# Kernel optimization log

Hardware: AMD Instinct MI355X
Metric: run time of the kernel (lower is better)

Reference implementation:

```python
import jax, jax.numpy as jnp
import numpy as np

N_NODES = 100000
N_EDGES = 1600000
N_GRAPHS = 128
BEHAVIOR_DIM = 32
LLM_DIM = 768
LLM_PROJ = 32
HIDDEN = 64
NUM_CLASSES = 2
INPUT_DIM = 64 + 16 + LLM_PROJ + BEHAVIOR_DIM  # 144


def gcn_conv(h, edge_index, edge_weight, W, b, n):
    """PyG GCNConv: linear -> gcn_norm with self-loops -> scatter-add at target."""
    h = h @ W  # [N, out]
    row, col = edge_index[0], edge_index[1]
    loop = jnp.arange(n)
    row_f = jnp.concatenate([row, loop])
    col_f = jnp.concatenate([col, loop])
    ew_f = jnp.concatenate([edge_weight, jnp.ones((n,), h.dtype)])
    deg = jax.ops.segment_sum(ew_f, col_f, num_segments=n)
    dinv = jnp.where(deg > 0, jax.lax.rsqrt(deg), 0.0)
    norm = dinv[row_f] * ew_f * dinv[col_f]  # [E+N]
    out = jax.ops.segment_sum(norm[:, None] * h[row_f], col_f, num_segments=n)
    return out + b


def global_mean_pool(x, batch, num_graphs):
    s = jax.ops.segment_sum(x, batch, num_segments=num_graphs)
    cnt = jax.ops.segment_sum(jnp.ones((x.shape[0],), x.dtype), batch, num_segments=num_graphs)
    return s / jnp.maximum(cnt, 1.0)[:, None]


def setup_inputs() -> dict:
    key = jax.random.key(0)
    ks = jax.random.split(key, 16)
    inp = {
        "x_names": jax.random.randint(ks[0], (N_NODES,), 0, 20000),
        "x_types": jax.random.randint(ks[1], (N_NODES,), 0, 100),
        "x_behaviors": jax.random.normal(ks[2], (N_NODES, BEHAVIOR_DIM), jnp.float32),
        "edge_index": jax.random.randint(ks[3], (2, N_EDGES), 0, N_NODES),
        "edge_weight": jax.random.uniform(ks[4], (N_EDGES,), jnp.float32),
        "batch": jnp.sort(jax.random.randint(ks[5], (N_NODES,), 0, N_GRAPHS)),
        "llm_features": jax.random.normal(ks[6], (N_NODES, LLM_DIM), jnp.float32),
        # parameters
        "name_emb": jax.random.normal(ks[7], (20000, 64), jnp.float32),
        "type_emb": jax.random.normal(ks[8], (100, 16), jnp.float32),
        "llm_proj_w": jax.random.normal(ks[9], (LLM_DIM, LLM_PROJ), jnp.float32) * 0.02,
        "llm_proj_b": jnp.zeros((LLM_PROJ,), jnp.float32),
        "conv1_w": jax.random.normal(ks[10], (INPUT_DIM, HIDDEN), jnp.float32) * 0.08,
        "conv1_b": jnp.zeros((HIDDEN,), jnp.float32),
        "conv2_w": jax.random.normal(ks[11], (HIDDEN, HIDDEN), jnp.float32) * 0.12,
        "conv2_b": jnp.zeros((HIDDEN,), jnp.float32),
        "cls_w": jax.random.normal(ks[12], (HIDDEN, NUM_CLASSES), jnp.float32) * 0.12,
        "cls_b": jnp.zeros((NUM_CLASSES,), jnp.float32),
    }
    return inp


def reference(x_names, x_types, x_behaviors, edge_index, edge_weight, batch,
              llm_features, name_emb, type_emb, llm_proj_w, llm_proj_b,
              conv1_w, conv1_b, conv2_w, conv2_b, cls_w, cls_b):
    n = x_names.shape[0]
    name_feat = name_emb[x_names]          # [N, 64]
    type_feat = type_emb[x_types]          # [N, 16]
    llm_feat = llm_features @ llm_proj_w + llm_proj_b  # [N, 32]
    x = jnp.concatenate([name_feat, type_feat, llm_feat, x_behaviors], axis=1)
    # dropout is identity in eval mode
    x = jax.nn.relu(gcn_conv(x, edge_index, edge_weight, conv1_w, conv1_b, n))
    x = jax.nn.relu(gcn_conv(x, edge_index, edge_weight, conv2_w, conv2_b, n))
    x = global_mean_pool(x, batch, N_GRAPHS)  # [G, HIDDEN]
    return x @ cls_w + cls_b                   # [G, 2]
```

## Files before the change

### kernel.cpp

```cpp
#include <hip/hip_runtime.h>
#include <cstdint>
#include <cstddef>

typedef __attribute__((ext_vector_type(8))) short bf16x8;
typedef __attribute__((ext_vector_type(4))) float f32x4;


__device__ __forceinline__ unsigned bf_rne(float x) {
  unsigned u = __float_as_uint(x);
  return (u + 0x7FFFu + ((u >> 16) & 1u)) >> 16;
}

__device__ __forceinline__ void split1(float x, short& hi, short& lo) {
  unsigned hb = bf_rne(x);
  hi = (short)hb;
  float fh = __uint_as_float(hb << 16);
  lo = (short)bf_rne(x - fh);
}

__device__ __forceinline__ void split8(const float4& p, const float4& q, bf16x8& h, bf16x8& l) {
  short hh, ll;
  split1(p.x, hh, ll); h[0] = hh; l[0] = ll;
  split1(p.y, hh, ll); h[1] = hh; l[1] = ll;
  split1(p.z, hh, ll); h[2] = hh; l[2] = ll;
  split1(p.w, hh, ll); h[3] = hh; l[3] = ll;
  split1(q.x, hh, ll); h[4] = hh; l[4] = ll;
  split1(q.y, hh, ll); h[5] = hh; l[5] = ll;
  split1(q.z, hh, ll); h[6] = hh; l[6] = ll;
  split1(q.w, hh, ll); h[7] = hh; l[7] = ll;
}


__global__ void prep1_kernel(const float* __restrict__ pw, const float* __restrict__ pb,
                             const float* __restrict__ w1,
                             short* __restrict__ Bh, short* __restrict__ Bl,
                             float* __restrict__ biasf) {
  int idx = blockIdx.x * 256 + threadIdx.x;
  if (idx < 896 * 64) {
    int gk = idx >> 6, col = idx & 63;
    float val;
    if (gk < 768) {
      float acc = 0.0f;
      #pragma unroll 8
      for (int m = 0; m < 32; ++m) acc = fmaf(pw[gk * 32 + m], w1[(80 + m) * 64 + col], acc);
      val = acc;
    } else if (gk < 832) val = w1[(gk - 768) * 64 + col];
    else if (gk < 848)   val = w1[(64 + gk - 832) * 64 + col];
    else if (gk < 864)   val = w1[(112 + gk - 848) * 64 + col];
    else if (gk < 880)   val = w1[(128 + gk - 864) * 64 + col];
    else                 val = 0.0f;
    int chunk = gk >> 5, k = gk & 31;
    int g, j;
    if (k < 16) { g = k >> 2; j = k & 3; } else { int k2 = k - 16; g = k2 >> 2; j = 4 + (k2 & 3); }
    size_t o = ((size_t)(chunk * 4 + g) * 64 + col) * 8 + j;
    short hh, ll; split1(val, hh, ll);
    Bh[o] = hh; Bl[o] = ll;
  } else if (idx < 896 * 64 + 64) {
    int col = idx - 896 * 64;
    float acc = 0.0f;
    for (int m = 0; m < 32; ++m) acc = fmaf(pb[m], w1[(80 + m) * 64 + col], acc);
    biasf[col] = acc;
  }
}

__global__ void prep2_kernel(const float* __restrict__ w2,
                             short* __restrict__ B2h, short* __restrict__ B2l) {
  int idx = blockIdx.x * 256 + threadIdx.x;
  if (idx >= 64 * 64) return;
  int gk = idx >> 6, col = idx & 63;
  float val = w2[gk * 64 + col];
  int chunk = gk >> 5, k = gk & 31;
  int g, j;
  if (k < 16) { g = k >> 2; j = k & 3; } else { int k2 = k - 16; g = k2 >> 2; j = 4 + (k2 & 3); }
  size_t o = ((size_t)(chunk * 4 + g) * 64 + col) * 8 + j;
  short hh, ll; split1(val, hh, ll);
  B2h[o] = hh; B2l[o] = ll;
}


__global__ void cnt_kernel(const int* __restrict__ ei, int* __restrict__ cnt, int E) {
  int e = blockIdx.x * 256 + threadIdx.x;
  if (e < E) atomicAdd(&cnt[ei[E + e]], 1);
}

__global__ __launch_bounds__(256) void scan_blk(const int* __restrict__ cnt,
                                                int* __restrict__ colp,
                                                int* __restrict__ bsum, int n) {
  __shared__ int ws[4];
  int t = threadIdx.x, lane = t & 63, w = t >> 6;
  int i = blockIdx.x * 256 + t;
  int v = (i < n) ? cnt[i] : 0;
  int x = v;
  #pragma unroll
  for (int off = 1; off < 64; off <<= 1) { int y = __shfl_up(x, off); if (lane >= off) x += y; }
  if (lane == 63) ws[w] = x;
  __syncthreads();
  if (t == 0) {
    int s = 0;
    #pragma unroll
    for (int k = 0; k < 4; ++k) { int tmp = ws[k]; ws[k] = s; s += tmp; }
    bsum[blockIdx.x] = s;
  }
  __syncthreads();
  if (i < n) colp[i] = ws[w] + x - v;
}

__global__ __launch_bounds__(512) void scan_top(int* __restrict__ bsum,
                                                int* __restrict__ colp, int nb, int n) {
  __shared__ int ws[8];
  int t = threadIdx.x, lane = t & 63, w = t >> 6;
  int v = (t < nb) ? bsum[t] : 0;
  int x = v;
  #pragma unroll
  for (int off = 1; off < 64; off <<= 1) { int y = __shfl_up(x, off); if (lane >= off) x += y; }
  if (lane == 63) ws[w] = x;
  __syncthreads();
  if (t == 0) {
    int s = 0;
    #pragma unroll
    for (int k = 0; k < 8; ++k) { int tmp = ws[k]; ws[k] = s; s += tmp; }
  }
  __syncthreads();
  int excl = ws[w] + x - v;
  if (t < nb) bsum[t] = excl;
  if (t == nb - 1) colp[n] = excl + v;
}

__global__ void scan_add(int* __restrict__ colp, int* __restrict__ fillp,
                         const int* __restrict__ bsum, int n) {
  int i = blockIdx.x * 256 + threadIdx.x;
  if (i < n) {
    int c = colp[i] + bsum[blockIdx.x];
    colp[i] = c;
    fillp[i] = c;
  }
}

__global__ void fill_kernel(const int* __restrict__ ei, const float* __restrict__ ew,
                            int* __restrict__ fillp, int2* __restrict__ csr, int E) {
  int e = blockIdx.x * 256 + threadIdx.x;
  if (e >= E) return;
  int row = ei[e], col = ei[E + e];
  int pos = atomicAdd(&fillp[col], 1);
  csr[pos] = make_int2(row, __float_as_int(ew[e]));
}

__global__ void degsum_kernel(const int* __restrict__ colp, const int2* __restrict__ csr,
                              float* __restrict__ dinv, int n) {
  int j = blockIdx.x * 256 + threadIdx.x;
  if (j >= n) return;
  int e0 = colp[j], e1 = colp[j + 1];
  float s = 1.0f;
  for (int e = e0; e < e1; ++e) s += __int_as_float(csr[e].y);
  dinv[j] = rsqrtf(s);
}

__global__ void wfix_kernel(int2* __restrict__ csr, const float* __restrict__ dinv, int E) {
  int i = blockIdx.x * 256 + threadIdx.x;
  if (i >= E) return;
  int2 m = csr[i];
  csr[i] = make_int2(m.x, __float_as_int(__int_as_float(m.y) * dinv[m.x]));
}


__device__ __forceinline__ void mfma24(f32x4 (&acc)[2][4],
                                       const bf16x8& ah0, const bf16x8& al0,
                                       const bf16x8& ah1, const bf16x8& al1,
                                       const bf16x8 (&bh)[4], const bf16x8 (&bl)[4]) {
  #pragma unroll
  for (int ct = 0; ct < 4; ++ct) {
    acc[0][ct] = __builtin_amdgcn_mfma_f32_16x16x32_bf16(ah0, bh[ct], acc[0][ct], 0, 0, 0);
    acc[0][ct] = __builtin_amdgcn_mfma_f32_16x16x32_bf16(ah0, bl[ct], acc[0][ct], 0, 0, 0);
    acc[0][ct] = __builtin_amdgcn_mfma_f32_16x16x32_bf16(al0, bh[ct], acc[0][ct], 0, 0, 0);
  }
  #pragma unroll
  for (int ct = 0; ct < 4; ++ct) {
    acc[1][ct] = __builtin_amdgcn_mfma_f32_16x16x32_bf16(ah1, bh[ct], acc[1][ct], 0, 0, 0);
    acc[1][ct] = __builtin_amdgcn_mfma_f32_16x16x32_bf16(ah1, bl[ct], acc[1][ct], 0, 0, 0);
    acc[1][ct] = __builtin_amdgcn_mfma_f32_16x16x32_bf16(al1, bh[ct], acc[1][ct], 0, 0, 0);
  }
}

__device__ __forceinline__ void loadB(const short* __restrict__ Bh, const short* __restrict__ Bl,
                                      int c, int g, int r16, bf16x8 (&bh)[4], bf16x8 (&bl)[4]) {
  #pragma unroll
  for (int ct = 0; ct < 4; ++ct) {
    size_t o = ((size_t)(c * 4 + g) * 64 + ct * 16 + r16) * 8;
    bh[ct] = *(const bf16x8*)(Bh + o);
    bl[ct] = *(const bf16x8*)(Bl + o);
  }
}

__global__ __launch_bounds__(256, 3) void gemm1_kernel(
    const float* __restrict__ llm, const short* __restrict__ Bh, const short* __restrict__ Bl,
    const int* __restrict__ names, const int* __restrict__ types,
    const float* __restrict__ beh, const float* __restrict__ nemb,
    const float* __restrict__ temb, const float* __restrict__ biasf,
    float* __restrict__ out, int n)
{
  int nwg = gridDim.x;
  int b = blockIdx.x;
  int q = nwg >> 3, r = nwg & 7;
  int xcd = b & 7, idx = b >> 3;
  int swz = (xcd < r ? xcd * (q + 1) : r * (q + 1) + (xcd - r) * q) + idx;

  int w = swz * 4 + (threadIdx.x >> 6);
  int nw = (n + 31) >> 5;
  if (w >= nw) return;
  int lane = threadIdx.x & 63;
  int g = lane >> 4, r16 = lane & 15;
  int base = w * 32;

  int arow0 = base + r16;      if (arow0 > n - 1) arow0 = n - 1;
  int arow1 = base + 16 + r16; if (arow1 > n - 1) arow1 = n - 1;
  int nm0 = names[arow0], nm1 = names[arow1];
  int tp0 = types[arow0], tp1 = types[arow1];

  const float* pA0 = llm + (size_t)arow0 * 768 + g * 4;
  const float* pA1 = llm + (size_t)arow1 * 768 + g * 4;

  f32x4 acc[2][4];
  #pragma unroll
  for (int i = 0; i < 2; ++i)
    #pragma unroll
    for (int j = 0; j < 4; ++j) { acc[i][j][0] = 0.f; acc[i][j][1] = 0.f; acc[i][j][2] = 0.f; acc[i][j][3] = 0.f; }

  float4 X0l = *(const float4*)(pA0 +  0), X0h = *(const float4*)(pA0 + 16);
  float4 X1l = *(const float4*)(pA1 +  0), X1h = *(const float4*)(pA1 + 16);
  float4 Y0l = *(const float4*)(pA0 + 32), Y0h = *(const float4*)(pA0 + 48);
  float4 Y1l = *(const float4*)(pA1 + 32), Y1h = *(const float4*)(pA1 + 48);

  bf16x8 bh[4], bl[4], ah0, al0, ah1, al1;

  #pragma unroll 1
  for (int cc = 0; cc < 11; ++cc) {
    const int c = cc * 2;
    loadB(Bh, Bl, c, g, r16, bh, bl);
    split8(X0l, X0h, ah0, al0);
    split8(X1l, X1h, ah1, al1);
    X0l = *(const float4*)(pA0 + (c + 2) * 32);
    X0h = *(const float4*)(pA0 + (c + 2) * 32 + 16);
    X1l = *(const float4*)(pA1 + (c + 2) * 32);
    X1h = *(const float4*)(pA1 + (c + 2) * 32 + 16);
    mfma24(acc, ah0, al0, ah1, al1, bh, bl);
    loadB(Bh, Bl, c + 1, g, r16, bh, bl);
    split8(Y0l, Y0h, ah0, al0);
    split8(Y1l, Y1h, ah1, al1);
    Y0l = *(const float4*)(pA0 + (c + 3) * 32);
    Y0h = *(const float4*)(pA0 + (c + 3) * 32 + 16);
    Y1l = *(const float4*)(pA1 + (c + 3) * 32);
    Y1h = *(const float4*)(pA1 + (c + 3) * 32 + 16);
    mfma24(acc, ah0, al0, ah1, al1, bh, bl);
  }

  loadB(Bh, Bl, 22, g, r16, bh, bl);
  split8(X0l, X0h, ah0, al0);
  split8(X1l, X1h, ah1, al1);
  mfma24(acc, ah0, al0, ah1, al1, bh, bl);

  loadB(Bh, Bl, 23, g, r16, bh, bl);
  split8(Y0l, Y0h, ah0, al0);
  split8(Y1l, Y1h, ah1, al1);
  mfma24(acc, ah0, al0, ah1, al1, bh, bl);

  const float* pN0 = nemb + (size_t)nm0 * 64 + g * 4;
  const float* pN1 = nemb + (size_t)nm1 * 64 + g * 4;
  #pragma unroll
  for (int t = 0; t < 2; ++t) {
    float4 l0 = *(const float4*)(pN0 + t * 32), h0 = *(const float4*)(pN0 + t * 32 + 16);
    float4 l1 = *(const float4*)(pN1 + t * 32), h1 = *(const float4*)(pN1 + t * 32 + 16);
    loadB(Bh, Bl, 24 + t, g, r16, bh, bl);
    split8(l0, h0, ah0, al0);
    split8(l1, h1, ah1, al1);
    mfma24(acc, ah0, al0, ah1, al1, bh, bl);
  }
  {
    float4 l0 = *(const float4*)(temb + (size_t)tp0 * 16 + g * 4);
    float4 h0 = *(const float4*)(beh + (size_t)arow0 * 32 + g * 4);
    float4 l1 = *(const float4*)(temb + (size_t)tp1 * 16 + g * 4);
    float4 h1 = *(const float4*)(beh + (size_t)arow1 * 32 + g * 4);
    loadB(Bh, Bl, 26, g, r16, bh, bl);
    split8(l0, h0, ah0, al0);
    split8(l1, h1, ah1, al1);
    mfma24(acc, ah0, al0, ah1, al1, bh, bl);
  }
  {
    const float4 z = make_float4(0.f, 0.f, 0.f, 0.f);
    float4 l0 = *(const float4*)(beh + (size_t)arow0 * 32 + 16 + g * 4);
    float4 l1 = *(const float4*)(beh + (size_t)arow1 * 32 + 16 + g * 4);
    loadB(Bh, Bl, 27, g, r16, bh, bl);
    split8(l0, z, ah0, al0);
    split8(l1, z, ah1, al1);
    mfma24(acc, ah0, al0, ah1, al1, bh, bl);
  }

  #pragma unroll
  for (int ct = 0; ct < 4; ++ct) {
    int col = ct * 16 + r16;
    float bf = biasf[col];
    #pragma unroll
    for (int rr = 0; rr < 4; ++rr) {
      int node0 = base + g * 4 + rr;
      if (node0 < n) out[(size_t)node0 * 64 + col] = acc[0][ct][rr] + bf;
      int node1 = base + 16 + g * 4 + rr;
      if (node1 < n) out[(size_t)node1 * 64 + col] = acc[1][ct][rr] + bf;
    }
  }
}


__global__ __launch_bounds__(256, 4) void gemm2_kernel(
    const float* __restrict__ h, const short* __restrict__ B2h, const short* __restrict__ B2l,
    float* __restrict__ out, int n)
{
  int w = blockIdx.x * 4 + (threadIdx.x >> 6);
  int nw = (n + 31) >> 5;
  if (w >= nw) return;
  int lane = threadIdx.x & 63;
  int g = lane >> 4, r16 = lane & 15;
  int base = w * 32;
  int arow0 = base + r16;      if (arow0 > n - 1) arow0 = n - 1;
  int arow1 = base + 16 + r16; if (arow1 > n - 1) arow1 = n - 1;

  f32x4 acc[2][4];
  #pragma unroll
  for (int i = 0; i < 2; ++i)
    #pragma unroll
    for (int j = 0; j < 4; ++j) { acc[i][j][0] = 0.f; acc[i][j][1] = 0.f; acc[i][j][2] = 0.f; acc[i][j][3] = 0.f; }

  #pragma unroll
  for (int c = 0; c < 2; ++c) {
    bf16x8 bh[4], bl[4];
    loadB(B2h, B2l, c, g, r16, bh, bl);
    const float* p0 = h + (size_t)arow0 * 64 + c * 32 + g * 4;
    const float* p1 = h + (size_t)arow1 * 64 + c * 32 + g * 4;
    float4 lo0 = *(const float4*)p0, hi0 = *(const float4*)(p0 + 16);
    float4 lo1 = *(const float4*)p1, hi1 = *(const float4*)(p1 + 16);
    bf16x8 ah0, al0, ah1, al1;
    split8(lo0, hi0, ah0, al0);
    split8(lo1, hi1, ah1, al1);
    mfma24(acc, ah0, al0, ah1, al1, bh, bl);
  }

  #pragma unroll
  for (int ct = 0; ct < 4; ++ct) {
    int col = ct * 16 + r16;
    #pragma unroll
    for (int rr = 0; rr < 4; ++rr) {
      int node0 = base + g * 4 + rr;
      if (node0 < n) out[(size_t)node0 * 64 + col] = acc[0][ct][rr];
      int node1 = base + 16 + g * 4 + rr;
      if (node1 < n) out[(size_t)node1 * 64 + col] = acc[1][ct][rr];
    }
  }
}


__global__ __launch_bounds__(256) void agg_kernel(
    const float* __restrict__ h, const int* __restrict__ colp,
    const int2* __restrict__ csr, const float* __restrict__ dinv,
    const float* __restrict__ bias, float* __restrict__ out, int n)
{
  int wid = threadIdx.x >> 6, lane = threadIdx.x & 63;
  int j = blockIdx.x * 4 + wid;
  if (j >= n) return;
  float dj = dinv[j];
  float hj = h[(size_t)j * 64 + lane];
  int e0 = colp[j], e1 = colp[j + 1];
  float s = 0.0f;
  int e = e0;
  for (; e + 4 <= e1; e += 4) {
    int2 m0 = csr[e], m1 = csr[e + 1], m2 = csr[e + 2], m3 = csr[e + 3];
    float f0 = h[(size_t)m0.x * 64 + lane];
    float f1 = h[(size_t)m1.x * 64 + lane];
    float f2 = h[(size_t)m2.x * 64 + lane];
    float f3 = h[(size_t)m3.x * 64 + lane];
    s = fmaf(__int_as_float(m0.y), f0, s);
    s = fmaf(__int_as_float(m1.y), f1, s);
    s = fmaf(__int_as_float(m2.y), f2, s);
    s = fmaf(__int_as_float(m3.y), f3, s);
  }
  for (; e < e1; ++e) {
    int2 m = csr[e];
    s = fmaf(__int_as_float(m.y), h[(size_t)m.x * 64 + lane], s);
  }
  float acc = bias[lane] + dj * fmaf(dj, hj, s);
  out[(size_t)j * 64 + lane] = fmaxf(acc, 0.0f);
}


__global__ __launch_bounds__(256) void pool_kernel(const float* __restrict__ x,
                                                   const int* __restrict__ batch,
                                                   float* __restrict__ pooled, int n) {
  __shared__ float red[4][64];
  __shared__ int range_s[2];
  int gph = blockIdx.x;
  int tid = threadIdx.x, wid = tid >> 6, lane = tid & 63;
  if (tid < 2) {
    int target = gph + tid;
    int lo = 0, hi = n;
    while (lo < hi) { int m = (lo + hi) >> 1; if (batch[m] < target) lo = m + 1; else hi = m; }
    range_s[tid] = lo;
  }
  __syncthreads();
  int lo = range_s[0], hi = range_s[1];
  float acc = 0.0f;
  for (int i = lo + wid; i < hi; i += 4) acc += x[(size_t)i * 64 + lane];
  red[wid][lane] = acc;
  __syncthreads();
  if (tid < 64) {
    float sum = red[0][lane] + red[1][lane] + red[2][lane] + red[3][lane];
    float cntf = (float)(hi - lo);
    pooled[gph * 64 + lane] = sum / fmaxf(cntf, 1.0f);
  }
}

__global__ void cls_kernel(const float* __restrict__ pooled, const float* __restrict__ cw,
                           const float* __restrict__ cb, float* __restrict__ out) {
  int t = threadIdx.x;
  int gph = t >> 1, c = t & 1;
  float acc = cb[c];
  #pragma unroll 8
  for (int k = 0; k < 64; ++k) acc = fmaf(pooled[gph * 64 + k], cw[k * 2 + c], acc);
  out[gph * 2 + c] = acc;
}


extern "C" void kernel_launch(void* const* d_in, const int* in_sizes, int n_in,
                              void* d_out, int out_size, void* d_ws, size_t ws_size,
                              hipStream_t stream) {
  const int*   x_names  = (const int*)  d_in[0];
  const int*   x_types  = (const int*)  d_in[1];
  const float* behav    = (const float*)d_in[2];
  const int*   ei       = (const int*)  d_in[3];
  const float* ew       = (const float*)d_in[4];
  const int*   batch    = (const int*)  d_in[5];
  const float* llm      = (const float*)d_in[6];
  const float* name_emb = (const float*)d_in[7];
  const float* type_emb = (const float*)d_in[8];
  const float* pw       = (const float*)d_in[9];
  const float* pb       = (const float*)d_in[10];
  const float* w1       = (const float*)d_in[11];
  const float* b1       = (const float*)d_in[12];
  const float* w2       = (const float*)d_in[13];
  const float* b2       = (const float*)d_in[14];
  const float* cw       = (const float*)d_in[15];
  const float* cb       = (const float*)d_in[16];

  const int N = in_sizes[0];
  const int E = in_sizes[4];
  const int nb = (N + 255) / 256;
  const int eb = (E + 255) / 256;
  const int nwaves = (N + 31) / 32;
  const int gblocks = (nwaves + 3) / 4;

  char* p = (char*)d_ws;
  auto alloc = [&](size_t bytes) -> void* {
    void* r = (void*)p; p += (bytes + 255) & ~(size_t)255; return r;
  };
  float* dinv   = (float*)alloc((size_t)N * 4);
  int*   cnt    = (int*)  alloc((size_t)N * 4);
  int*   colp   = (int*)  alloc((size_t)(N + 1) * 4);
  int*   fillp  = (int*)  alloc((size_t)N * 4);
  int2*  csr    = (int2*) alloc((size_t)E * 8);
  int*   bsum   = (int*)  alloc((size_t)(nb + 1) * 4);
  short* Bh     = (short*)alloc((size_t)896 * 64 * 2);
  short* Bl     = (short*)alloc((size_t)896 * 64 * 2);
  short* B2h    = (short*)alloc((size_t)64 * 64 * 2);
  short* B2l    = (short*)alloc((size_t)64 * 64 * 2);
  float* biasf  = (float*)alloc((size_t)64 * 4);
  float* bufX   = (float*)alloc((size_t)N * 64 * 4);
  float* bufY   = (float*)alloc((size_t)N * 64 * 4);
  float* pooled = (float*)alloc((size_t)128 * 64 * 4);
  (void)ws_size; (void)n_in; (void)out_size;

  prep1_kernel<<<(896 * 64 + 64 + 255) / 256, 256, 0, stream>>>(pw, pb, w1, Bh, Bl, biasf);
  prep2_kernel<<<16, 256, 0, stream>>>(w2, B2h, B2l);
  hipMemsetAsync(cnt, 0, (size_t)N * 4, stream);
  cnt_kernel<<<eb, 256, 0, stream>>>(ei, cnt, E);
  scan_blk<<<nb, 256, 0, stream>>>(cnt, colp, bsum, N);
  scan_top<<<1, 512, 0, stream>>>(bsum, colp, nb, N);
  scan_add<<<nb, 256, 0, stream>>>(colp, fillp, bsum, N);
  fill_kernel<<<eb, 256, 0, stream>>>(ei, ew, fillp, csr, E);
  degsum_kernel<<<nb, 256, 0, stream>>>(colp, csr, dinv, N);
  wfix_kernel<<<eb, 256, 0, stream>>>(csr, dinv, E);

  gemm1_kernel<<<gblocks, 256, 0, stream>>>(llm, Bh, Bl, x_names, x_types, behav,
                                            name_emb, type_emb, biasf, bufX, N);
  agg_kernel<<<(N + 3) / 4, 256, 0, stream>>>(bufX, colp, csr, dinv, b1, bufY, N);
  gemm2_kernel<<<gblocks, 256, 0, stream>>>(bufY, B2h, B2l, bufX, N);
  agg_kernel<<<(N + 3) / 4, 256, 0, stream>>>(bufX, colp, csr, dinv, b2, bufY, N);
  pool_kernel<<<128, 256, 0, stream>>>(bufY, batch, pooled, N);
  cls_kernel<<<1, 256, 0, stream>>>(pooled, cw, cb, (float*)d_out);
}
```

Measured before the change: 548.2 us.

## Stage LLM tile through LDS with coalesced loads; fold degree into edge-count pass

gemm1 now has each 256-thread block cooperatively load a 64-row tile of llm features with fully coalesced float4 reads. It splits each value into bf16 hi/lo once and writes them into double-buffered, XOR-swizzled shared memory, so each wave computes 16 rows instead of 32. Separately, the degree sum is computed with float atomics during edge counting, and the source normalization is applied while filling the CSR. That drops the degsum and wfix passes over the CSR. The cost is float-atomic nondeterminism in the degree sum, more LDS use and lower occupancy in gemm1.

New measurement: 611.6 us. +11.6%, slower.

```diff
diff --git a/kernel.cpp b/kernel.cpp
--- a/kernel.cpp
+++ b/kernel.cpp
@@ -4,6 +4,10 @@
 
 typedef __attribute__((ext_vector_type(8))) short bf16x8;
 typedef __attribute__((ext_vector_type(4))) float f32x4;
+
+#define ROWSTR 40
+#define PLANE  (64 * ROWSTR)
+#define ABUF   (4 * PLANE)
 
 
 __device__ __forceinline__ unsigned bf_rne(float x) {
@@ -78,9 +82,23 @@
 }
 
 
-__global__ void cnt_kernel(const int* __restrict__ ei, int* __restrict__ cnt, int E) {
+__global__ void init_kernel(float* __restrict__ deg, int* __restrict__ cnt, int n) {
+  int i = blockIdx.x * 256 + threadIdx.x;
+  if (i < n) { deg[i] = 1.0f; cnt[i] = 0; }
+}
+
+__global__ void cnt_kernel(const int* __restrict__ ei, const float* __restrict__ ew,
+                           int* __restrict__ cnt, float* __restrict__ deg, int E) {
   int e = blockIdx.x * 256 + threadIdx.x;
-  if (e < E) atomicAdd(&cnt[ei[E + e]], 1);
+  if (e >= E) return;
+  int col = ei[E + e];
+  atomicAdd(&cnt[col], 1);
+  atomicAdd(&deg[col], ew[e]);
+}
+
+__global__ void dinv_kernel(float* __restrict__ deg, int n) {
+  int i = blockIdx.x * 256 + threadIdx.x;
+  if (i < n) deg[i] = rsqrtf(deg[i]);
 }
 
 __global__ __launch_bounds__(256) void scan_blk(const int* __restrict__ cnt,
@@ -137,49 +155,15 @@
 }
 
 __global__ void fill_kernel(const int* __restrict__ ei, const float* __restrict__ ew,
-                            int* __restrict__ fillp, int2* __restrict__ csr, int E) {
+                            const float* __restrict__ dinv, int* __restrict__ fillp,
+                            int2* __restrict__ csr, int E) {
   int e = blockIdx.x * 256 + threadIdx.x;
   if (e >= E) return;
   int row = ei[e], col = ei[E + e];
   int pos = atomicAdd(&fillp[col], 1);
-  csr[pos] = make_int2(row, __float_as_int(ew[e]));
-}
-
-__global__ void degsum_kernel(const int* __restrict__ colp, const int2* __restrict__ csr,
-                              float* __restrict__ dinv, int n) {
-  int j = blockIdx.x * 256 + threadIdx.x;
-  if (j >= n) return;
-  int e0 = colp[j], e1 = colp[j + 1];
-  float s = 1.0f;
-  for (int e = e0; e < e1; ++e) s += __int_as_float(csr[e].y);
-  dinv[j] = rsqrtf(s);
-}
-
-__global__ void wfix_kernel(int2* __restrict__ csr, const float* __restrict__ dinv, int E) {
-  int i = blockIdx.x * 256 + threadIdx.x;
-  if (i >= E) return;
-  int2 m = csr[i];
-  csr[i] = make_int2(m.x, __float_as_int(__int_as_float(m.y) * dinv[m.x]));
-}
-
-
-__device__ __forceinline__ void mfma24(f32x4 (&acc)[2][4],
-                                       const bf16x8& ah0, const bf16x8& al0,
-                                       const bf16x8& ah1, const bf16x8& al1,
-                                       const bf16x8 (&bh)[4], const bf16x8 (&bl)[4]) {
-  #pragma unroll
-  for (int ct = 0; ct < 4; ++ct) {
-    acc[0][ct] = __builtin_amdgcn_mfma_f32_16x16x32_bf16(ah0, bh[ct], acc[0][ct], 0, 0, 0);
-    acc[0][ct] = __builtin_amdgcn_mfma_f32_16x16x32_bf16(ah0, bl[ct], acc[0][ct], 0, 0, 0);
-    acc[0][ct] = __builtin_amdgcn_mfma_f32_16x16x32_bf16(al0, bh[ct], acc[0][ct], 0, 0, 0);
-  }
-  #pragma unroll
-  for (int ct = 0; ct < 4; ++ct) {
-    acc[1][ct] = __builtin_amdgcn_mfma_f32_16x16x32_bf16(ah1, bh[ct], acc[1][ct], 0, 0, 0);
-    acc[1][ct] = __builtin_amdgcn_mfma_f32_16x16x32_bf16(ah1, bl[ct], acc[1][ct], 0, 0, 0);
-    acc[1][ct] = __builtin_amdgcn_mfma_f32_16x16x32_bf16(al1, bh[ct], acc[1][ct], 0, 0, 0);
-  }
-}
+  csr[pos] = make_int2(row, __float_as_int(ew[e] * dinv[row]));
+}
+
 
 __device__ __forceinline__ void loadB(const short* __restrict__ Bh, const short* __restrict__ Bl,
                                       int c, int g, int r16, bf16x8 (&bh)[4], bf16x8 (&bl)[4]) {
@@ -191,107 +175,127 @@
   }
 }
 
-__global__ __launch_bounds__(256, 3) void gemm1_kernel(
+__device__ __forceinline__ void mfma12(f32x4 (&acc)[4], const bf16x8& ah, const bf16x8& al,
+                                       const bf16x8 (&bh)[4], const bf16x8 (&bl)[4]) {
+  #pragma unroll
+  for (int ct = 0; ct < 4; ++ct) {
+    acc[ct] = __builtin_amdgcn_mfma_f32_16x16x32_bf16(ah, bh[ct], acc[ct], 0, 0, 0);
+    acc[ct] = __builtin_amdgcn_mfma_f32_16x16x32_bf16(ah, bl[ct], acc[ct], 0, 0, 0);
+    acc[ct] = __builtin_amdgcn_mfma_f32_16x16x32_bf16(al, bh[ct], acc[ct], 0, 0, 0);
+  }
+}
+
+__global__ __launch_bounds__(256, 2) void gemm1_kernel(
     const float* __restrict__ llm, const short* __restrict__ Bh, const short* __restrict__ Bl,
     const int* __restrict__ names, const int* __restrict__ types,
     const float* __restrict__ beh, const float* __restrict__ nemb,
     const float* __restrict__ temb, const float* __restrict__ biasf,
     float* __restrict__ out, int n)
 {
+  __shared__ short Ah[2][ABUF];
+  __shared__ short Al[2][ABUF];
+
   int nwg = gridDim.x;
   int b = blockIdx.x;
   int q = nwg >> 3, r = nwg & 7;
-  int xcd = b & 7, idx = b >> 3;
-  int swz = (xcd < r ? xcd * (q + 1) : r * (q + 1) + (xcd - r) * q) + idx;
-
-  int w = swz * 4 + (threadIdx.x >> 6);
-  int nw = (n + 31) >> 5;
-  if (w >= nw) return;
-  int lane = threadIdx.x & 63;
-  int g = lane >> 4, r16 = lane & 15;
-  int base = w * 32;
-
-  int arow0 = base + r16;      if (arow0 > n - 1) arow0 = n - 1;
-  int arow1 = base + 16 + r16; if (arow1 > n - 1) arow1 = n - 1;
-  int nm0 = names[arow0], nm1 = names[arow1];
-  int tp0 = types[arow0], tp1 = types[arow1];
-
-  const float* pA0 = llm + (size_t)arow0 * 768 + g * 4;
-  const float* pA1 = llm + (size_t)arow1 * 768 + g * 4;
-
-  f32x4 acc[2][4];
-  #pragma unroll
-  for (int i = 0; i < 2; ++i)
+  int xcd = b & 7, bidx = b >> 3;
+  int swz = (xcd < r ? xcd * (q + 1) : r * (q + 1) + (xcd - r) * q) + bidx;
+
+  const int tid = threadIdx.x;
+  const int lane = tid & 63, wv = tid >> 6;
+  const int g = lane >> 4, r16 = lane & 15;
+  const int base = swz * 64;
+
+  const int colq = tid & 31;
+  const int rw8  = tid >> 5;
+  const int kc_s = colq >> 3;
+  const int qq   = colq & 7;
+  const int pos0 = (((qq & 3) * 8) + ((qq >> 2) * 4)) ^ (kc_s << 3);
+  const int wbase = kc_s * PLANE + rw8 * ROWSTR + pos0;
+
+  const float* rp[8];
+  #pragma unroll
+  for (int it = 0; it < 8; ++it) {
+    int grow = base + rw8 + it * 8;
+    if (grow > n - 1) grow = n - 1;
+    rp[it] = llm + (size_t)grow * 768 + colq * 4;
+  }
+
+  const int arowL = wv * 16 + r16;
+  int arowG = base + arowL;
+  if (arowG > n - 1) arowG = n - 1;
+  const int nm = names[arowG], tp = types[arowG];
+
+  f32x4 acc[4];
+  #pragma unroll
+  for (int ct = 0; ct < 4; ++ct) { acc[ct][0] = 0.f; acc[ct][1] = 0.f; acc[ct][2] = 0.f; acc[ct][3] = 0.f; }
+
+  float4 sv[8];
+  #pragma unroll
+  for (int it = 0; it < 8; ++it) sv[it] = *(const float4*)(rp[it]);
+  #pragma unroll
+  for (int it = 0; it < 8; ++it) {
+    short4 h4, l4;
+    split1(sv[it].x, h4.x, l4.x); split1(sv[it].y, h4.y, l4.y);
+    split1(sv[it].z, h4.z, l4.z); split1(sv[it].w, h4.w, l4.w);
+    *(short4*)&Ah[0][wbase + it * 8 * ROWSTR] = h4;
+    *(short4*)&Al[0][wbase + it * 8 * ROWSTR] = l4;
+  }
+  __syncthreads();
+
+  int cur = 0;
+  #pragma unroll 1
+  for (int i = 0; i < 6; ++i) {
+    if (i < 5) {
+      #pragma unroll
+      for (int it = 0; it < 8; ++it) sv[it] = *(const float4*)(rp[it] + (i + 1) * 128);
+    }
+    __builtin_amdgcn_sched_barrier(0);
     #pragma unroll
-    for (int j = 0; j < 4; ++j) { acc[i][j][0] = 0.f; acc[i][j][1] = 0.f; acc[i][j][2] = 0.f; acc[i][j][3] = 0.f; }
-
-  float4 X0l = *(const float4*)(pA0 +  0), X0h = *(const float4*)(pA0 + 16);
-  float4 X1l = *(const float4*)(pA1 +  0), X1h = *(const float4*)(pA1 + 16);
-  float4 Y0l = *(const float4*)(pA0 + 32), Y0h = *(const float4*)(pA0 + 48);
-  float4 Y1l = *(const float4*)(pA1 + 32), Y1h = *(const float4*)(pA1 + 48);
-
-  bf16x8 bh[4], bl[4], ah0, al0, ah1, al1;
-
-  #pragma unroll 1
-  for (int cc = 0; cc < 11; ++cc) {
-    const int c = cc * 2;
-    loadB(Bh, Bl, c, g, r16, bh, bl);
-    split8(X0l, X0h, ah0, al0);
-    split8(X1l, X1h, ah1, al1);
-    X0l = *(const float4*)(pA0 + (c + 2) * 32);
-    X0h = *(const float4*)(pA0 + (c + 2) * 32 + 16);
-    X1l = *(const float4*)(pA1 + (c + 2) * 32);
-    X1h = *(const float4*)(pA1 + (c + 2) * 32 + 16);
-    mfma24(acc, ah0, al0, ah1, al1, bh, bl);
-    loadB(Bh, Bl, c + 1, g, r16, bh, bl);
-    split8(Y0l, Y0h, ah0, al0);
-    split8(Y1l, Y1h, ah1, al1);
-    Y0l = *(const float4*)(pA0 + (c + 3) * 32);
-    Y0h = *(const float4*)(pA0 + (c + 3) * 32 + 16);
-    Y1l = *(const float4*)(pA1 + (c + 3) * 32);
-    Y1h = *(const float4*)(pA1 + (c + 3) * 32 + 16);
-    mfma24(acc, ah0, al0, ah1, al1, bh, bl);
-  }
-
-  loadB(Bh, Bl, 22, g, r16, bh, bl);
-  split8(X0l, X0h, ah0, al0);
-  split8(X1l, X1h, ah1, al1);
-  mfma24(acc, ah0, al0, ah1, al1, bh, bl);
-
-  loadB(Bh, Bl, 23, g, r16, bh, bl);
-  split8(Y0l, Y0h, ah0, al0);
-  split8(Y1l, Y1h, ah1, al1);
-  mfma24(acc, ah0, al0, ah1, al1, bh, bl);
-
-  const float* pN0 = nemb + (size_t)nm0 * 64 + g * 4;
-  const float* pN1 = nemb + (size_t)nm1 * 64 + g * 4;
+    for (int kc = 0; kc < 4; ++kc) {
+      bf16x8 bh[4], bl[4];
+      loadB(Bh, Bl, i * 4 + kc, g, r16, bh, bl);
+      int ro = kc * PLANE + arowL * ROWSTR + ((g ^ kc) * 8);
+      bf16x8 ah = *(const bf16x8*)&Ah[cur][ro];
+      bf16x8 al = *(const bf16x8*)&Al[cur][ro];
+      mfma12(acc, ah, al, bh, bl);
+    }
+    if (i < 5) {
+      #pragma unroll
+      for (int it = 0; it < 8; ++it) {
+        short4 h4, l4;
+        split1(sv[it].x, h4.x, l4.x); split1(sv[it].y, h4.y, l4.y);
+        split1(sv[it].z, h4.z, l4.z); split1(sv[it].w, h4.w, l4.w);
+        *(short4*)&Ah[cur ^ 1][wbase + it * 8 * ROWSTR] = h4;
+        *(short4*)&Al[cur ^ 1][wbase + it * 8 * ROWSTR] = l4;
+      }
+    }
+    __syncthreads();
+    cur ^= 1;
+  }
+
+  bf16x8 bh[4], bl[4], ah, al;
+  const float* pN = nemb + (size_t)nm * 64 + g * 4;
   #pragma unroll
   for (int t = 0; t < 2; ++t) {
-    float4 l0 = *(const float4*)(pN0 + t * 32), h0 = *(const float4*)(pN0 + t * 32 + 16);
-    float4 l1 = *(const float4*)(pN1 + t * 32), h1 = *(const float4*)(pN1 + t * 32 + 16);
+    float4 l = *(const float4*)(pN + t * 32), h = *(const float4*)(pN + t * 32 + 16);
     loadB(Bh, Bl, 24 + t, g, r16, bh, bl);
-    split8(l0, h0, ah0, al0);
-    split8(l1, h1, ah1, al1);
-    mfma24(acc, ah0, al0, ah1, al1, bh, bl);
+    split8(l, h, ah, al);
+    mfma12(acc, ah, al, bh, bl);
   }
   {
-    float4 l0 = *(const float4*)(temb + (size_t)tp0 * 16 + g * 4);
-    float4 h0 = *(const float4*)(beh + (size_t)arow0 * 32 + g * 4);
-    float4 l1 = *(const float4*)(temb + (size_t)tp1 * 16 + g * 4);
-    float4 h1 = *(const float4*)(beh + (size_t)arow1 * 32 + g * 4);
+    float4 l = *(const float4*)(temb + (size_t)tp * 16 + g * 4);
+    float4 h = *(const float4*)(beh + (size_t)arowG * 32 + g * 4);
     loadB(Bh, Bl, 26, g, r16, bh, bl);
-    split8(l0, h0, ah0, al0);
-    split8(l1, h1, ah1, al1);
-    mfma24(acc, ah0, al0, ah1, al1, bh, bl);
+    split8(l, h, ah, al);
+    mfma12(acc, ah, al, bh, bl);
   }
   {
     const float4 z = make_float4(0.f, 0.f, 0.f, 0.f);
-    float4 l0 = *(const float4*)(beh + (size_t)arow0 * 32 + 16 + g * 4);
-    float4 l1 = *(const float4*)(beh + (size_t)arow1 * 32 + 16 + g * 4);
+    float4 l = *(const float4*)(beh + (size_t)arowG * 32 + 16 + g * 4);
     loadB(Bh, Bl, 27, g, r16, bh, bl);
-    split8(l0, z, ah0, al0);
-    split8(l1, z, ah1, al1);
-    mfma24(acc, ah0, al0, ah1, al1, bh, bl);
+    split8(l, z, ah, al);
+    mfma12(acc, ah, al, bh, bl);
   }
 
   #pragma unroll
@@ -300,14 +304,30 @@
     float bf = biasf[col];
     #pragma unroll
     for (int rr = 0; rr < 4; ++rr) {
-      int node0 = base + g * 4 + rr;
-      if (node0 < n) out[(size_t)node0 * 64 + col] = acc[0][ct][rr] + bf;
-      int node1 = base + 16 + g * 4 + rr;
-      if (node1 < n) out[(size_t)node1 * 64 + col] = acc[1][ct][rr] + bf;
+      int node = base + wv * 16 + g * 4 + rr;
+      if (node < n) out[(size_t)node * 64 + col] = acc[ct][rr] + bf;
     }
   }
 }
 
+
+__device__ __forceinline__ void mfma24(f32x4 (&acc)[2][4],
+                                       const bf16x8& ah0, const bf16x8& al0,
+                                       const bf16x8& ah1, const bf16x8& al1,
+                                       const bf16x8 (&bh)[4], const bf16x8 (&bl)[4]) {
+  #pragma unroll
+  for (int ct = 0; ct < 4; ++ct) {
+    acc[0][ct] = __builtin_amdgcn_mfma_f32_16x16x32_bf16(ah0, bh[ct], acc[0][ct], 0, 0, 0);
+    acc[0][ct] = __builtin_amdgcn_mfma_f32_16x16x32_bf16(ah0, bl[ct], acc[0][ct], 0, 0, 0);
+    acc[0][ct] = __builtin_amdgcn_mfma_f32_16x16x32_bf16(al0, bh[ct], acc[0][ct], 0, 0, 0);
+  }
+  #pragma unroll
+  for (int ct = 0; ct < 4; ++ct) {
+    acc[1][ct] = __builtin_amdgcn_mfma_f32_16x16x32_bf16(ah1, bh[ct], acc[1][ct], 0, 0, 0);
+    acc[1][ct] = __builtin_amdgcn_mfma_f32_16x16x32_bf16(ah1, bl[ct], acc[1][ct], 0, 0, 0);
+    acc[1][ct] = __builtin_amdgcn_mfma_f32_16x16x32_bf16(al1, bh[ct], acc[1][ct], 0, 0, 0);
+  }
+}
 
 __global__ __launch_bounds__(256, 4) void gemm2_kernel(
     const float* __restrict__ h, const short* __restrict__ B2h, const short* __restrict__ B2l,
@@ -451,8 +471,8 @@
   const int E = in_sizes[4];
   const int nb = (N + 255) / 256;
   const int eb = (E + 255) / 256;
-  const int nwaves = (N + 31) / 32;
-  const int gblocks = (nwaves + 3) / 4;
+  const int g1blocks = (N + 63) / 64;
+  const int g2blocks = ((N + 31) / 32 + 3) / 4;
 
   char* p = (char*)d_ws;
   auto alloc = [&](size_t bytes) -> void* {
@@ -474,21 +494,20 @@
   float* pooled = (float*)alloc((size_t)128 * 64 * 4);
   (void)ws_size; (void)n_in; (void)out_size;
 
+  init_kernel<<<nb, 256, 0, stream>>>(dinv, cnt, N);
   prep1_kernel<<<(896 * 64 + 64 + 255) / 256, 256, 0, stream>>>(pw, pb, w1, Bh, Bl, biasf);
   prep2_kernel<<<16, 256, 0, stream>>>(w2, B2h, B2l);
-  hipMemsetAsync(cnt, 0, (size_t)N * 4, stream);
-  cnt_kernel<<<eb, 256, 0, stream>>>(ei, cnt, E);
+  cnt_kernel<<<eb, 256, 0, stream>>>(ei, ew, cnt, dinv, E);
+  dinv_kernel<<<nb, 256, 0, stream>>>(dinv, N);
   scan_blk<<<nb, 256, 0, stream>>>(cnt, colp, bsum, N);
   scan_top<<<1, 512, 0, stream>>>(bsum, colp, nb, N);
   scan_add<<<nb, 256, 0, stream>>>(colp, fillp, bsum, N);
-  fill_kernel<<<eb, 256, 0, stream>>>(ei, ew, fillp, csr, E);
-  degsum_kernel<<<nb, 256, 0, stream>>>(colp, csr, dinv, N);
-  wfix_kernel<<<eb, 256, 0, stream>>>(csr, dinv, E);
-
-  gemm1_kernel<<<gblocks, 256, 0, stream>>>(llm, Bh, Bl, x_names, x_types, behav,
-                                            name_emb, type_emb, biasf, bufX, N);
+  fill_kernel<<<eb, 256, 0, stream>>>(ei, ew, dinv, fillp, csr, E);
+
+  gemm1_kernel<<<g1blocks, 256, 0, stream>>>(llm, Bh, Bl, x_names, x_types, behav,
+                                             name_emb, type_emb, biasf, bufX, N);
   agg_kernel<<<(N + 3) / 4, 256, 0, stream>>>(bufX, colp, csr, dinv, b1, bufY, N);
-  gemm2_kernel<<<gblocks, 256, 0, stream>>>(bufY, B2h, B2l, bufX, N);
+  gemm2_kernel<<<g2blocks, 256, 0, stream>>>(bufY, B2h, B2l, bufX, N);
   agg_kernel<<<(N + 3) / 4, 256, 0, stream>>>(bufX, colp, csr, dinv, b2, bufY, N);
   pool_kernel<<<128, 256, 0, stream>>>(bufY, batch, pooled, N);
   cls_kernel<<<1, 256, 0, stream>>>(pooled, cw, cb, (float*)d_out);
```
